# Kernel tuning notes

Hardware: AMD Instinct MI355X
Metric: run time of the kernel (lower is better)

## Reference

```python
import math
import jax, jax.numpy as jnp
import numpy as np
from jax.scipy.special import erf, erfinv, logsumexp

M = 250000          # number of (u, v) datapoints
P = 4               # n_phases
N_MC = 64           # MC samples per interface pair
IA, IB = np.triu_indices(P, 1)   # interface pair indices (Ia < Ib since I is increasing)
K = len(IA)                      # n_interfaces = 6
LOG2 = math.log(2.0)
LOG2PI = math.log(2.0 * math.pi)
LOG_GAMMA_3_2 = math.log(math.gamma(1.5))


def _logsinh(x):
    # numerically stable log(sinh(x)); x > 0 in all uses here
    s = jnp.abs(x)
    return -LOG2 + s + jnp.log1p(-jnp.exp(-2.0 * s))


def _log_bessel_05(x):
    # I_{1/2}(x) = sqrt(2/(pi x)) sinh(x)
    return 0.5 * LOG2 - 0.5 * jnp.log(math.pi * x) + _logsinh(x)


def setup_inputs() -> dict:
    key = jax.random.key(0)
    k0, k1, k2 = jax.random.split(key, 3)
    u = jax.random.uniform(k0, (M,), dtype=jnp.float32)                 # intensities in [0,1]
    v = jax.random.uniform(k1, (M,), dtype=jnp.float32) * 0.3 + 0.01    # gradient magnitudes > 0
    eps = jax.random.uniform(k2, (K, N_MC), dtype=jnp.float32)          # fresh MC draw per interface
    I = jnp.linspace(0.0, 1.0, P, dtype=jnp.float32)
    W = jnp.zeros((K + P,), dtype=jnp.float32)
    sigma_b = jnp.array([2.0], dtype=jnp.float32)
    sigma_n = jnp.array([0.1], dtype=jnp.float32)
    d = jnp.array([2.0], dtype=jnp.float32)
    r = jnp.array([0.05], dtype=jnp.float32)
    return {"u": u, "v": v, "eps": eps, "I": I, "W": W,
            "sigma_b": sigma_b, "sigma_n": sigma_n, "d": d, "r": r}


def reference(u, v, eps, I, W, sigma_b, sigma_n, d, r):
    sb = sigma_b[0]
    sn = sigma_n[0]
    dd = d[0]
    rho = jnp.tanh(r[0])
    sr = sn * jnp.sqrt(1.0 - rho)          # sigma_n * sqrt(1 - rho)
    s2 = sn ** 2 * (1.0 - rho)
    N = eps.shape[1]
    log_w = jax.nn.log_softmax(W)

    # interior phases: [P, M]
    interior = (LOG2 + 2.0 * jnp.log(v) - LOG_GAMMA_3_2 - 3.0 * jnp.log(sr)
                - (v / sr) ** 2 - jnp.log(sn) - 0.5 * LOG2PI
                - 0.5 * ((u - I[:, None]) / sn) ** 2)

    rows = [interior]
    log_v = jnp.log(v)
    v2 = v ** 2
    for k in range(K):  # small fixed loop over interface pairs
        Ia = I[IA[k]]
        Ib = I[IB[k]]
        x = eps[k] * 2.0 * dd * sb - dd * sb                              # [N]
        In = (erf(x / (math.sqrt(2.0) * sb)) + 1.0) * 0.5 * (Ib - Ia) + Ia  # [N]
        # log p(u | I): [N, M]
        lu = -jnp.log(sn) - 0.5 * LOG2PI - 0.5 * ((u[None, :] - In[:, None]) / sn) ** 2
        # G(I): [N]
        Gk = (Ib - Ia) / jnp.sqrt(2.0 * math.pi * sb ** 2) * jnp.exp(
            -erfinv(2.0 * (In - Ia) / (Ib - Ia) - 1.0) ** 2)
        # log p(v | I): [N, M]
        lb = _log_bessel_05(2.0 * v[None, :] * Gk[:, None] / s2)
        lv = (LOG2 - 2.0 * jnp.log(sr) + 1.5 * log_v[None, :]
              - 0.5 * jnp.log(Gk)[:, None] + lb
              - (v2[None, :] + Gk[:, None] ** 2) / s2)
        rows.append((-math.log(N) + logsumexp(lu + lv, axis=0))[None, :])

    log_p = jnp.concatenate(rows, axis=0)                 # [P + K, M]
    log_p_uv = logsumexp(log_w[:, None] + log_p, axis=0)  # [M]
    return -jnp.sum(log_p_uv) / u.shape[0]
```

## Files before the change

### kernel.cpp

```cpp
#include <hip/hip_runtime.h>
#include <math.h>

#define KN 384
#define TPB 256

__device__ float  g_tx[KN], g_ty[KN], g_tz[KN];
__device__ float  g_hdr[12];
__device__ double g_part[1024];
__device__ int    g_ctr = 0;

__device__ __forceinline__ float fexp2(float x) {
  return __builtin_amdgcn_exp2f(x);
}

__global__ __launch_bounds__(KN) void prep_kernel(
    const float* __restrict__ eps, const float* __restrict__ I,
    const float* __restrict__ W, const float* __restrict__ sb_,
    const float* __restrict__ sn_, const float* __restrict__ d_,
    const float* __restrict__ r_) {
  const int t = threadIdx.x;
  const float sb  = sb_[0];
  const float sn  = sn_[0];
  const float dd  = d_[0];
  const float rho = tanhf(r_[0]);
  const float s2  = sn * sn * (1.f - rho);
  const float sr  = sqrtf(s2);
  const float isn = 1.f / sn;
  const float inv_s2 = 1.f / s2;
  const float LOG2E = 1.4426950408889634f;
  const float SQH   = sqrtf(0.5f * LOG2E);

  float wmax = W[0];
  for (int j = 1; j < 10; ++j) wmax = fmaxf(wmax, W[j]);
  float se = 0.f;
  for (int j = 0; j < 10; ++j) se += expf(W[j] - wmax);
  const float lse = wmax + logf(se);

  const float LOG2PI_ = 1.8378770664093453f;
  const float LOG2_   = 0.6931471805599453f;
  const float LGG32   = -0.12078223763524522f;
  const float LOGPI_  = 1.1447298858494002f;
  const float Cterm = -logf(sn) - 0.5f * LOG2PI_ - logf(sr) - 0.5f * LOGPI_;
  const float Cint0 = LOG2_ - LGG32 - 3.f * logf(sr) - logf(sn) - 0.5f * LOG2PI_;

  if (t < 12) {
    float h = 0.f;
    if      (t == 0) h = isn * SQH;
    else if (t == 1) h = inv_s2 * LOG2E;
    else if (t < 6)  h = I[t - 2] * isn * SQH;
    else if (t < 10) h = expf(W[t - 6] - lse + Cint0);
    g_hdr[t] = h;
  }

  const int IAc[6] = {0, 0, 0, 1, 1, 2};
  const int IBc[6] = {1, 2, 3, 2, 3, 3};
  const int k = t >> 6;
  const float Ia = I[IAc[k]], Ib = I[IBc[k]];
  const float wk = expf(W[4 + k] - lse + Cterm) * (1.0f / 64.0f);
  const float e  = eps[t];
  const float x  = e * 2.f * dd * sb - dd * sb;
  const float y  = x / (1.4142135623730951f * sb);
  const float In = (erff(y) + 1.f) * 0.5f * (Ib - Ia) + Ia;
  const float qq = 2.f * (In - Ia) / (Ib - Ia) - 1.f;
  const float gi = erfinvf(qq);
  const float G  = (Ib - Ia) * 0.3989422804014327f / sb * expf(-gi * gi);
  g_tx[t] = In * isn * SQH;
  g_ty[t] = 2.f * inv_s2 * G * LOG2E;
  g_tz[t] = wk * expf(-G * G * inv_s2) / G;
}

__global__ __launch_bounds__(TPB, 4) void main_kernel(
    const float* __restrict__ u, const float* __restrict__ v,
    float* __restrict__ out, int M, int nb) {
  __shared__ double red[TPB];
  __shared__ int    slast;
  const int tid = threadIdx.x;
  const int i   = blockIdx.x * TPB + tid;

  float uu = 0.f, vv = 1.f;
  if (i < M) { uu = u[i]; vv = v[i]; }

  const float husc = g_hdr[0];
  const float hg   = g_hdr[1];

  const float us = uu * husc;
  const float gg = fexp2(-vv * vv * hg);
  float aint = 0.f;
#pragma unroll
  for (int p = 0; p < 4; ++p) {
    const float dq = us - g_hdr[2 + p];
    aint = fmaf(g_hdr[6 + p], fexp2(-dq * dq), aint);
  }
  const float c0 = (i < M) ? vv * gg : 0.f;
  const float c1 = (i < M) ? vv * vv * gg * aint : 1.f;

  float S0 = 0.f, S1 = 0.f, S2 = 0.f, S3 = 0.f;
  float S4 = 0.f, S5 = 0.f, S6 = 0.f, S7 = 0.f;
#define ENT(TX, TY, TZ, S)                         \
  {                                                \
    const float du = us - (TX);                    \
    const float nd = du * -du;                     \
    const float a1 = fmaf(vv, (TY), nd);           \
    const float a2 = fmaf(vv, -(TY), nd);          \
    S = fmaf((TZ), fexp2(a1), S);                  \
    S = fmaf(-(TZ), fexp2(a2), S);                 \
  }
#pragma unroll 6
  for (int g = 0; g < KN / 8; ++g) {
    const int b = g * 8;
    float X[8], Y[8], Z[8];
#pragma unroll
    for (int j = 0; j < 8; ++j) {
      X[j] = g_tx[b + j];
      Y[j] = g_ty[b + j];
      Z[j] = g_tz[b + j];
    }
    ENT(X[0], Y[0], Z[0], S0) ENT(X[1], Y[1], Z[1], S1)
    ENT(X[2], Y[2], Z[2], S2) ENT(X[3], Y[3], Z[3], S3)
    ENT(X[4], Y[4], Z[4], S4) ENT(X[5], Y[5], Z[5], S5)
    ENT(X[6], Y[6], Z[6], S6) ENT(X[7], Y[7], Z[7], S7)
  }
#undef ENT
  const float S = ((S0 + S1) + (S2 + S3)) + ((S4 + S5) + (S6 + S7));

  double mysum = (double)__logf(fmaf(c0, S, c1));

  red[tid] = mysum;
  __syncthreads();
  for (int s = TPB / 2; s > 0; s >>= 1) {
    if (tid < s) red[tid] += red[tid + s];
    __syncthreads();
  }
  if (tid == 0)
    __hip_atomic_store(&g_part[blockIdx.x], red[0], __ATOMIC_RELAXED,
                       __HIP_MEMORY_SCOPE_AGENT);

  if (tid == 0) {
    const int c = __hip_atomic_fetch_add(&g_ctr, 1, __ATOMIC_ACQ_REL,
                                         __HIP_MEMORY_SCOPE_AGENT);
    slast = (c == nb - 1) ? 1 : 0;
  }
  __syncthreads();
  if (slast) {
    double s = 0.0;
    for (int j = tid; j < nb; j += TPB)
      s += __hip_atomic_load(&g_part[j], __ATOMIC_RELAXED,
                             __HIP_MEMORY_SCOPE_AGENT);
    red[tid] = s;
    __syncthreads();
    for (int k2 = TPB / 2; k2 > 0; k2 >>= 1) {
      if (tid < k2) red[tid] += red[tid + k2];
      __syncthreads();
    }
    if (tid == 0) {
      out[0] = (float)(-red[0] / (double)M);
      __hip_atomic_store(&g_ctr, 0, __ATOMIC_RELAXED,
                         __HIP_MEMORY_SCOPE_AGENT);
    }
  }
}

extern "C" void kernel_launch(void* const* d_in, const int* in_sizes, int n_in,
                              void* d_out, int out_size, void* d_ws, size_t ws_size,
                              hipStream_t stream) {
  const float* u   = (const float*)d_in[0];
  const float* v   = (const float*)d_in[1];
  const float* eps = (const float*)d_in[2];
  const float* I   = (const float*)d_in[3];
  const float* W   = (const float*)d_in[4];
  const float* sb  = (const float*)d_in[5];
  const float* sn  = (const float*)d_in[6];
  const float* dd  = (const float*)d_in[7];
  const float* r   = (const float*)d_in[8];
  const int M  = in_sizes[0];
  const int nb = (M + TPB - 1) / TPB;

  hipLaunchKernelGGL(prep_kernel, dim3(1), dim3(KN), 0, stream,
                     eps, I, W, sb, sn, dd, r);
  hipLaunchKernelGGL(main_kernel, dim3(nb), dim3(TPB), 0, stream,
                     u, v, (float*)d_out, M, nb);
}
```

Baseline: 105.4 us.

## Split per-point MC sum across two half-blocks to double grid parallelism

Each block now handles 128 points, with the two halves of the block each summing half of the 384 precomputed MC table entries. Partial sums are combined through shared memory before the log, and only the second half computes the interior-phase terms. This doubles the number of blocks and shortens each block, aiming to improve occupancy and reduce tail imbalance across CUs. It adds a shared-memory exchange, a barrier, and twice as many partial results in the final reduction.

```diff
diff --git a/kernel.cpp b/kernel.cpp
--- a/kernel.cpp
+++ b/kernel.cpp
@@ -3,10 +3,11 @@
 
 #define KN 384
 #define TPB 256
+#define PPB 128
 
 __device__ float  g_tx[KN], g_ty[KN], g_tz[KN];
 __device__ float  g_hdr[12];
-__device__ double g_part[1024];
+__device__ double g_part[2048];
 __device__ int    g_ctr = 0;
 
 __device__ __forceinline__ float fexp2(float x) {
@@ -69,31 +70,41 @@
   g_tz[t] = wk * expf(-G * G * inv_s2) / G;
 }
 
-__global__ __launch_bounds__(TPB, 4) void main_kernel(
+__global__ __launch_bounds__(TPB, 8) void main_kernel(
     const float* __restrict__ u, const float* __restrict__ v,
     float* __restrict__ out, int M, int nb) {
+  __shared__ float  sS[PPB];
   __shared__ double red[TPB];
   __shared__ int    slast;
   const int tid = threadIdx.x;
-  const int i   = blockIdx.x * TPB + tid;
+  const int pi  = tid & (PPB - 1);
+  const int hu  = __builtin_amdgcn_readfirstlane(tid >> 7);
+  const int i   = blockIdx.x * PPB + pi;
+  const bool act = i < M;
 
   float uu = 0.f, vv = 1.f;
-  if (i < M) { uu = u[i]; vv = v[i]; }
+  if (act) { uu = u[i]; vv = v[i]; }
 
   const float husc = g_hdr[0];
   const float hg   = g_hdr[1];
+  const float us   = uu * husc;
 
-  const float us = uu * husc;
-  const float gg = fexp2(-vv * vv * hg);
-  float aint = 0.f;
+  float c0 = 0.f, c1 = 1.f;
+  if (hu == 1 && act) {
+    const float gg = fexp2(-vv * vv * hg);
+    float aint = 0.f;
 #pragma unroll
-  for (int p = 0; p < 4; ++p) {
-    const float dq = us - g_hdr[2 + p];
-    aint = fmaf(g_hdr[6 + p], fexp2(-dq * dq), aint);
+    for (int p = 0; p < 4; ++p) {
+      const float dq = us - g_hdr[2 + p];
+      aint = fmaf(g_hdr[6 + p], fexp2(-dq * dq), aint);
+    }
+    c0 = vv * gg;
+    c1 = vv * vv * gg * aint;
   }
-  const float c0 = (i < M) ? vv * gg : 0.f;
-  const float c1 = (i < M) ? vv * vv * gg * aint : 1.f;
 
+  const float* ptx = g_tx + hu * (KN / 2);
+  const float* pty = g_ty + hu * (KN / 2);
+  const float* ptz = g_tz + hu * (KN / 2);
   float S0 = 0.f, S1 = 0.f, S2 = 0.f, S3 = 0.f;
   float S4 = 0.f, S5 = 0.f, S6 = 0.f, S7 = 0.f;
 #define ENT(TX, TY, TZ, S)                         \
@@ -106,14 +117,14 @@
     S = fmaf(-(TZ), fexp2(a2), S);                 \
   }
 #pragma unroll 6
-  for (int g = 0; g < KN / 8; ++g) {
+  for (int g = 0; g < KN / 16; ++g) {
     const int b = g * 8;
     float X[8], Y[8], Z[8];
 #pragma unroll
     for (int j = 0; j < 8; ++j) {
-      X[j] = g_tx[b + j];
-      Y[j] = g_ty[b + j];
-      Z[j] = g_tz[b + j];
+      X[j] = ptx[b + j];
+      Y[j] = pty[b + j];
+      Z[j] = ptz[b + j];
     }
     ENT(X[0], Y[0], Z[0], S0) ENT(X[1], Y[1], Z[1], S1)
     ENT(X[2], Y[2], Z[2], S2) ENT(X[3], Y[3], Z[3], S3)
@@ -121,9 +132,15 @@
     ENT(X[6], Y[6], Z[6], S6) ENT(X[7], Y[7], Z[7], S7)
   }
 #undef ENT
-  const float S = ((S0 + S1) + (S2 + S3)) + ((S4 + S5) + (S6 + S7));
+  const float Sh = ((S0 + S1) + (S2 + S3)) + ((S4 + S5) + (S6 + S7));
 
-  double mysum = (double)__logf(fmaf(c0, S, c1));
+  if (hu == 0) sS[pi] = Sh;
+  __syncthreads();
+  double mysum = 0.0;
+  if (hu == 1) {
+    const float S = sS[pi] + Sh;
+    mysum = (double)__logf(fmaf(c0, S, c1));
+  }
 
   red[tid] = mysum;
   __syncthreads();
@@ -173,7 +190,7 @@
   const float* dd  = (const float*)d_in[7];
   const float* r   = (const float*)d_in[8];
   const int M  = in_sizes[0];
-  const int nb = (M + TPB - 1) / TPB;
+  const int nb = (M + PPB - 1) / PPB;
 
   hipLaunchKernelGGL(prep_kernel, dim3(1), dim3(KN), 0, stream,
                      eps, I, W, sb, sn, dd, r);
```

Measured after the change: 112.6 us. +6.8%, slower.
